# Kernel optimization log

Hardware: AMD Instinct MI355X
Metric: run time of the kernel (lower is better)

Reference implementation:

```python
import jax, jax.numpy as jnp
import numpy as np

N = 4096
SPECIES = 100
FEA = 64        # atom_emb_dim
NBR_FEA = 64    # num gaussians
MAX_NBRS = 12
LN_EPS = 1e-5

# GaussianSmearing constants: linspace(0, 8, 64)
_OFFSET = jnp.linspace(0.0, 8.0, NBR_FEA)
_COEFF = -0.5 / float(8.0 / (NBR_FEA - 1)) ** 2


def _uniform(key, shape, fan_in):
    s = 1.0 / np.sqrt(fan_in)
    return jax.random.uniform(key, shape, minval=-s, maxval=s, dtype=jnp.float32)


def setup_inputs() -> dict:
    key = jax.random.key(0)
    ks = jax.random.split(key, 20)
    lat_pred = jnp.eye(3, dtype=jnp.float32) * 8.0 + 0.2 * jax.random.normal(ks[0], (3, 3), dtype=jnp.float32)
    fracs_pred = jax.random.uniform(ks[1], (N, 3), dtype=jnp.float32)
    species_logits = jax.random.normal(ks[2], (N, SPECIES), dtype=jnp.float32)
    occ_logits = jax.random.normal(ks[3], (N,), dtype=jnp.float32)
    # params
    emb_w = _uniform(ks[4], (SPECIES, FEA), SPECIES)
    emb_b = _uniform(ks[5], (FEA,), SPECIES)
    in1 = 2 * FEA + NBR_FEA  # 192
    w1 = _uniform(ks[6], (in1, 2 * FEA), in1)
    b1 = _uniform(ks[7], (2 * FEA,), in1)
    g1 = jnp.ones((2 * FEA,), jnp.float32)
    be1 = jnp.zeros((2 * FEA,), jnp.float32)
    w2 = _uniform(ks[8], (in1, 2 * FEA), in1)
    b2 = _uniform(ks[9], (2 * FEA,), in1)
    g2 = jnp.ones((2 * FEA,), jnp.float32)
    be2 = jnp.zeros((2 * FEA,), jnp.float32)
    fc_w = _uniform(ks[10], (FEA, 1), FEA)
    fc_b = _uniform(ks[11], (1,), FEA)
    return dict(lat_pred=lat_pred, fracs_pred=fracs_pred, species_logits=species_logits,
                occ_logits=occ_logits, emb_w=emb_w, emb_b=emb_b,
                w1=w1, b1=b1, g1=g1, be1=be1, w2=w2, b2=b2, g2=g2, be2=be2,
                fc_w=fc_w, fc_b=fc_b)


def _layernorm(x, g, b):
    m = jnp.mean(x, axis=-1, keepdims=True)
    v = jnp.var(x, axis=-1, keepdims=True)
    return (x - m) * jax.lax.rsqrt(v + LN_EPS) * g + b


def _cgcnn_layer(atom, nbr_atom, nbr_fea, w, b, g, be):
    # atom: [N,F]; nbr_atom: [N,M,F]; nbr_fea: [N,M,K]
    n, m = nbr_atom.shape[:2]
    atom_exp = jnp.broadcast_to(atom[:, None, :], (n, m, atom.shape[-1]))
    total = jnp.concatenate([atom_exp, nbr_atom, nbr_fea], axis=2)  # [N,M,2F+K]
    z = _layernorm(total @ w + b, g, be)                            # [N,M,2F]
    nbr_filter, nbr_core = jnp.split(z, 2, axis=2)
    nbr_sumed = jnp.sum(jax.nn.sigmoid(nbr_filter) * jax.nn.softplus(nbr_core), axis=1)
    return jax.nn.softplus(atom + nbr_sumed)


def reference(lat_pred, fracs_pred, species_logits, occ_logits,
              emb_w, emb_b, w1, b1, g1, be1, w2, b2, g2, be2, fc_w, fc_b):
    species_probs = jax.nn.softmax(species_logits, axis=-1)
    atom_fea = species_probs @ emb_w + emb_b                         # [N,F]
    diff = fracs_pred[:, None, :] - fracs_pred[None, :, :]           # [N,N,3]
    diff = diff - jnp.round(diff)                                    # min-image
    cart = diff @ lat_pred                                           # [N,N,3]
    dist = jnp.linalg.norm(cart, axis=-1)                            # [N,N]
    dist = dist + jnp.eye(dist.shape[0], dtype=dist.dtype) * 100.0
    k = min(MAX_NBRS, dist.shape[1] - 1)
    neg_d, nbr_idx = jax.lax.top_k(-dist, k)                         # smallest k
    nbr_dist = -neg_d                                                # [N,k]
    nbr_fea = jnp.exp(_COEFF * (nbr_dist[..., None] - _OFFSET) ** 2) # [N,k,K]
    nbr_atom_fea = atom_fea[nbr_idx]                                 # [N,k,F]
    atom_fea = _cgcnn_layer(atom_fea, nbr_atom_fea, nbr_fea, w1, b1, g1, be1)
    atom_fea = _cgcnn_layer(atom_fea, nbr_atom_fea, nbr_fea, w2, b2, g2, be2)
    occ_probs = jax.nn.sigmoid(occ_logits)[:, None]                  # [N,1]
    graph_fea = jnp.sum(atom_fea * occ_probs, axis=0) / (jnp.sum(occ_probs) + 1e-6)
    return graph_fea @ fc_w + fc_b                                   # [1]
```

## Files before the change

### kernel.cpp

```cpp
#include <hip/hip_runtime.h>
#include <math.h>

#define N_ATOMS 4096
#define SPECIES 100
#define FEA 64
#define M_NBR 12

typedef unsigned short u16;
typedef __attribute__((ext_vector_type(8))) _Float16 f16x8;
typedef __attribute__((ext_vector_type(4))) float f32x4;

constexpr float LN_EPS = 1e-5f;
constexpr float GAUSS_COEFF = -31.0078125f;
constexpr float D2_INF = 3.4e38f;

__device__ __forceinline__ float sigmoidf_(float x){
    return __fdividef(1.0f, 1.0f + __expf(-x));
}
__device__ __forceinline__ float softplusf_(float x){
    return fmaxf(x, 0.0f) + __logf(1.0f + __expf(-fabsf(x)));
}
__device__ __forceinline__ u16 f16bits(_Float16 h){ return *(u16*)&h; }

__global__ __launch_bounds__(256) void k_setup(const float* __restrict__ fracs,
        const float* __restrict__ w1, const float* __restrict__ w2,
        const float* __restrict__ logits, const float* __restrict__ emb_w,
        const float* __restrict__ emb_b,
        float* __restrict__ fx, float* __restrict__ fy, float* __restrict__ fz,
        u16* __restrict__ wpk, float* __restrict__ atom0, u16* __restrict__ a0f){
    __shared__ float sE[4][SPECIES];
    int b = blockIdx.x, t = threadIdx.x;
    if (b < 192){
        int gid = b * 256 + t;
        int layer = gid / 24576;
        int e = gid % 24576;
        int k = e >> 7, n = e & 127;
        float x = (layer ? w2 : w1)[e];
        int mat = layer * 3 + (k >> 6);
        int kk = k & 63;
        int ch = kk >> 5, lg2 = (kk >> 3) & 3, i = kk & 7;
        int nt = n >> 4, lr2 = n & 15;
        wpk[mat * 8192 + ((ch * 8 + nt) * 64 + (lg2 * 16 + lr2)) * 8 + i] = f16bits((_Float16)x);
    } else if (b < 208){
        int j = (b - 192) * 256 + t;
        fx[j] = fracs[j*3+0];
        fy[j] = fracs[j*3+1];
        fz[j] = fracs[j*3+2];
    } else {
        int grp = t >> 6, f = t & 63;
        int a = (b - 208) * 4 + grp;
        const float* lg = logits + (long)a * SPECIES;
        float l0 = lg[f];
        float l1 = (f + 64 < SPECIES) ? lg[f + 64] : -1e30f;
        float mx = fmaxf(l0, l1);
        #pragma unroll
        for (int off = 32; off; off >>= 1) mx = fmaxf(mx, __shfl_xor(mx, off));
        float e0 = __expf(l0 - mx);
        float e1 = (f + 64 < SPECIES) ? __expf(l1 - mx) : 0.0f;
        sE[grp][f] = e0;
        if (f + 64 < SPECIES) sE[grp][64 + f] = e1;
        float sm = e0 + e1;
        #pragma unroll
        for (int off = 32; off; off >>= 1) sm += __shfl_xor(sm, off);
        __syncthreads();
        float acc = 0.0f;
        for (int s = 0; s < SPECIES; ++s) acc += sE[grp][s] * emb_w[s * FEA + f];
        float v = acc / sm + emb_b[f];
        atom0[(long)a * FEA + f] = v;
        a0f[a * FEA + f] = f16bits((_Float16)v);
    }
}

__global__ __launch_bounds__(256) void k_topk(const float* __restrict__ fx,
        const float* __restrict__ fy, const float* __restrict__ fz,
        const float* __restrict__ lat, int* __restrict__ nbr_idx,
        float* __restrict__ nbr_dist){
    __shared__ int   hist[256];
    __shared__ int   cnt;
    __shared__ float sThr;
    __shared__ float candD[256];
    __shared__ int   candI[256];
    int i = blockIdx.x, tid = threadIdx.x;
    hist[tid] = 0;
    if (tid == 0) cnt = 0;
    __syncthreads();
    float l00=lat[0],l01=lat[1],l02=lat[2];
    float l10=lat[3],l11=lat[4],l12=lat[5];
    float l20=lat[6],l21=lat[7],l22=lat[8];
    float xi = fx[i], yi = fy[i], zi = fz[i];
    float d2r[16];
    #pragma unroll
    for (int k = 0; k < 16; ++k){
        int j = tid + k * 256;
        float dx = xi - fx[j];
        float dy = yi - fy[j];
        float dz = zi - fz[j];
        dx -= rintf(dx); dy -= rintf(dy); dz -= rintf(dz);
        float cx = dx*l00 + dy*l10 + dz*l20;
        float cy = dx*l01 + dy*l11 + dz*l21;
        float cz = dx*l02 + dy*l12 + dz*l22;
        float d2 = cx*cx + cy*cy + cz*cz;
        if (j == i) d2 = D2_INF;
        d2r[k] = d2;
        if (d2 < 4.0f) atomicAdd(&hist[(int)(d2 * 64.0f)], 1);
    }
    __syncthreads();
    if (tid < 64){
        int s0 = hist[4*tid] + hist[4*tid+1] + hist[4*tid+2] + hist[4*tid+3];
        int sc = s0;
        #pragma unroll
        for (int off = 1; off < 64; off <<= 1){
            int o = __shfl_up(sc, off);
            if (tid >= off) sc += o;
        }
        unsigned long long mball = __ballot(sc >= M_NBR);
        if (mball == 0ULL){
            if (tid == 0) sThr = 1e30f;
        } else {
            int gbin = __ffsll(mball) - 1;
            if (tid == gbin){
                int c = sc - s0;
                float th = 4.0f;
                #pragma unroll
                for (int b = 0; b < 4; ++b){
                    c += hist[4*gbin + b];
                    if (c >= M_NBR){ th = (float)(4*gbin + b + 1) * (1.0f/64.0f); break; }
                }
                sThr = th;
            }
        }
    }
    __syncthreads();
    float thr = sThr;
    #pragma unroll
    for (int k = 0; k < 16; ++k){
        if (d2r[k] < thr){
            int p = atomicAdd(&cnt, 1);
            if (p < 256){ candD[p] = d2r[k]; candI[p] = tid + k * 256; }
        }
    }
    __syncthreads();
    int n = cnt < 256 ? cnt : 256;
    for (int c = tid; c < n; c += 256){
        float dv = candD[c]; int iv = candI[c];
        int rank = 0;
        for (int s = 0; s < n; ++s){
            float ds_ = candD[s]; int is_ = candI[s];
            rank += (ds_ < dv || (ds_ == dv && is_ < iv)) ? 1 : 0;
        }
        if (rank < M_NBR){
            nbr_idx[i * M_NBR + rank]  = iv;
            nbr_dist[i * M_NBR + rank] = sqrtf(dv);
        }
    }
}

__global__ __launch_bounds__(192) void k_fused(
        const float* __restrict__ atom0F, const u16* __restrict__ a0f,
        const int* __restrict__ nbr_idx, const float* __restrict__ nbr_dist,
        const u16* __restrict__ wpk,
        const float* __restrict__ b1, const float* __restrict__ g1, const float* __restrict__ be1,
        const float* __restrict__ b2, const float* __restrict__ g2, const float* __restrict__ be2,
        float* __restrict__ outF)
{
    __shared__ float sS1w[3][4][132];
    __shared__ float sS2w[3][4][132];
    __shared__ float prod[48][68];
    __shared__ float sSF[4][64];
    __shared__ u16   sSH[4][64];

    const int t = threadIdx.x;
    const int w = t >> 6, l = t & 63;
    const int lg = l >> 4, lr = l & 15;
    const int blk = blockIdx.x;
    const int row = blk * 48 + w * 16 + lr;

    const int nid = nbr_idx[row];
    f16x8 nfr[2];
    nfr[0] = *(const f16x8*)(a0f + nid * 64 + lg * 8);
    nfr[1] = *(const f16x8*)(a0f + nid * 64 + 32 + lg * 8);

    f16x8 saf[2];
    #pragma unroll
    for (int c = 0; c < 2; ++c)
        saf[c] = (lr < 4) ? *(const f16x8*)(a0f + (blk * 4 + lr) * 64 + c * 32 + lg * 8)
                          : (f16x8)0;

    const float* a0flat = atom0F + (long)blk * 256;
    float res0 = a0flat[t];
    float res1 = (t < 64) ? a0flat[192 + t] : 0.0f;

    float g1v[8], be1v[8];
    #pragma unroll
    for (int nt = 0; nt < 8; ++nt){
        int c = nt * 16 + lr;
        g1v[nt] = g1[c]; be1v[nt] = be1[c];
    }

    const float dist = nbr_dist[row];
    f16x8 ga[2];
    #pragma unroll
    for (int c = 0; c < 2; ++c)
        #pragma unroll
        for (int i = 0; i < 8; ++i){
            int k = c * 32 + lg * 8 + i;
            float dd = dist - (float)k * (8.0f / 63.0f);
            ga[c][i] = (_Float16)__expf(GAUSS_COEFF * dd * dd);
        }

    int aloc[4];
    #pragma unroll
    for (int rr = 0; rr < 4; ++rr)
        aloc[rr] = (w * 16 + lg * 4 + rr) / 12;

    const u16* ws1 = wpk;
    const u16* wn1 = wpk + 1 * 8192;
    const u16* wg1 = wpk + 2 * 8192;
    const u16* ws2 = wpk + 3 * 8192;
    const u16* wn2 = wpk + 4 * 8192;
    const u16* wg2 = wpk + 5 * 8192;

    {
        f32x4 a1[8];
        #pragma unroll
        for (int nt = 0; nt < 8; ++nt) a1[nt] = 0.0f;
        #pragma unroll
        for (int c = 0; c < 2; ++c)
            #pragma unroll
            for (int nt = 0; nt < 8; ++nt){
                const f16x8 b = *(const f16x8*)(ws1 + ((c * 8 + nt) * 64 + l) * 8);
                a1[nt] = __builtin_amdgcn_mfma_f32_16x16x32_f16(saf[c], b, a1[nt], 0, 0, 0);
            }
        if (lg == 0){
            #pragma unroll
            for (int nt = 0; nt < 8; ++nt)
                #pragma unroll
                for (int rr = 0; rr < 4; ++rr)
                    sS1w[w][rr][nt * 16 + lr] = a1[nt][rr] + b1[nt * 16 + lr];
        }
    }

    f32x4 acc[8];
    #pragma unroll
    for (int nt = 0; nt < 8; ++nt) acc[nt] = 0.0f;
    #pragma unroll
    for (int c = 0; c < 2; ++c)
        #pragma unroll
        for (int nt = 0; nt < 8; ++nt){
            const f16x8 bn = *(const f16x8*)(wn1 + ((c * 8 + nt) * 64 + l) * 8);
            acc[nt] = __builtin_amdgcn_mfma_f32_16x16x32_f16(nfr[c], bn, acc[nt], 0, 0, 0);
            const f16x8 bg = *(const f16x8*)(wg1 + ((c * 8 + nt) * 64 + l) * 8);
            acc[nt] = __builtin_amdgcn_mfma_f32_16x16x32_f16(ga[c], bg, acc[nt], 0, 0, 0);
        }

    {
        float s[4] = {0,0,0,0}, q[4] = {0,0,0,0};
        #pragma unroll
        for (int nt = 0; nt < 8; ++nt)
            #pragma unroll
            for (int rr = 0; rr < 4; ++rr){
                float v = acc[nt][rr] + sS1w[w][aloc[rr]][nt * 16 + lr];
                acc[nt][rr] = v;
                s[rr] += v; q[rr] += v * v;
            }
        #pragma unroll
        for (int rr = 0; rr < 4; ++rr){
            #pragma unroll
            for (int m = 1; m < 16; m <<= 1){
                s[rr] += __shfl_xor(s[rr], m);
                q[rr] += __shfl_xor(q[rr], m);
            }
        }
        #pragma unroll
        for (int rr = 0; rr < 4; ++rr){
            float mean = s[rr] * (1.0f / 128.0f);
            float var  = q[rr] * (1.0f / 128.0f) - mean * mean;
            float inv  = rsqrtf(var + LN_EPS);
            #pragma unroll
            for (int nt = 0; nt < 4; ++nt){
                float zf = (acc[nt][rr]     - mean) * inv * g1v[nt]     + be1v[nt];
                float zc = (acc[nt + 4][rr] - mean) * inv * g1v[nt + 4] + be1v[nt + 4];
                prod[w * 16 + lg * 4 + rr][nt * 16 + lr] = sigmoidf_(zf) * softplusf_(zc);
            }
        }
    }
    __syncthreads();

    {
        int a_ = t >> 6, c = t & 63;
        float sm = 0.0f;
        #pragma unroll
        for (int m = 0; m < 12; ++m) sm += prod[a_ * 12 + m][c];
        float o = softplusf_(res0 + sm);
        sSF[a_][c] = o;
        sSH[a_][c] = f16bits((_Float16)o);
        if (t < 64){
            float sm2 = 0.0f;
            #pragma unroll
            for (int m = 0; m < 12; ++m) sm2 += prod[36 + m][c];
            float o2 = softplusf_(res1 + sm2);
            sSF[3][c] = o2;
            sSH[3][c] = f16bits((_Float16)o2);
        }
    }
    __syncthreads();

    float g2v[8], be2v[8];
    #pragma unroll
    for (int nt = 0; nt < 8; ++nt){
        int c = nt * 16 + lr;
        g2v[nt] = g2[c]; be2v[nt] = be2[c];
    }

    {
        f16x8 af[2];
        #pragma unroll
        for (int c = 0; c < 2; ++c)
            af[c] = (lr < 4) ? *(const f16x8*)(&sSH[lr][c * 32 + lg * 8]) : (f16x8)0;
        f32x4 a2[8];
        #pragma unroll
        for (int nt = 0; nt < 8; ++nt) a2[nt] = 0.0f;
        #pragma unroll
        for (int c = 0; c < 2; ++c)
            #pragma unroll
            for (int nt = 0; nt < 8; ++nt){
                const f16x8 b = *(const f16x8*)(ws2 + ((c * 8 + nt) * 64 + l) * 8);
                a2[nt] = __builtin_amdgcn_mfma_f32_16x16x32_f16(af[c], b, a2[nt], 0, 0, 0);
            }
        if (lg == 0){
            #pragma unroll
            for (int nt = 0; nt < 8; ++nt)
                #pragma unroll
                for (int rr = 0; rr < 4; ++rr)
                    sS2w[w][rr][nt * 16 + lr] = a2[nt][rr] + b2[nt * 16 + lr];
        }
    }

    f32x4 acc2[8];
    #pragma unroll
    for (int nt = 0; nt < 8; ++nt) acc2[nt] = 0.0f;
    #pragma unroll
    for (int c = 0; c < 2; ++c)
        #pragma unroll
        for (int nt = 0; nt < 8; ++nt){
            const f16x8 bn = *(const f16x8*)(wn2 + ((c * 8 + nt) * 64 + l) * 8);
            acc2[nt] = __builtin_amdgcn_mfma_f32_16x16x32_f16(nfr[c], bn, acc2[nt], 0, 0, 0);
            const f16x8 bg = *(const f16x8*)(wg2 + ((c * 8 + nt) * 64 + l) * 8);
            acc2[nt] = __builtin_amdgcn_mfma_f32_16x16x32_f16(ga[c], bg, acc2[nt], 0, 0, 0);
        }

    {
        float s[4] = {0,0,0,0}, q[4] = {0,0,0,0};
        #pragma unroll
        for (int nt = 0; nt < 8; ++nt)
            #pragma unroll
            for (int rr = 0; rr < 4; ++rr){
                float v = acc2[nt][rr] + sS2w[w][aloc[rr]][nt * 16 + lr];
                acc2[nt][rr] = v;
                s[rr] += v; q[rr] += v * v;
            }
        #pragma unroll
        for (int rr = 0; rr < 4; ++rr){
            #pragma unroll
            for (int m = 1; m < 16; m <<= 1){
                s[rr] += __shfl_xor(s[rr], m);
                q[rr] += __shfl_xor(q[rr], m);
            }
        }
        #pragma unroll
        for (int rr = 0; rr < 4; ++rr){
            float mean = s[rr] * (1.0f / 128.0f);
            float var  = q[rr] * (1.0f / 128.0f) - mean * mean;
            float inv  = rsqrtf(var + LN_EPS);
            #pragma unroll
            for (int nt = 0; nt < 4; ++nt){
                float zf = (acc2[nt][rr]     - mean) * inv * g2v[nt]     + be2v[nt];
                float zc = (acc2[nt + 4][rr] - mean) * inv * g2v[nt + 4] + be2v[nt + 4];
                prod[w * 16 + lg * 4 + rr][nt * 16 + lr] = sigmoidf_(zf) * softplusf_(zc);
            }
        }
    }
    __syncthreads();

    {
        int a_ = t >> 6, c = t & 63;
        float sm = 0.0f;
        #pragma unroll
        for (int m = 0; m < 12; ++m) sm += prod[a_ * 12 + m][c];
        outF[(long)blk * 256 + t] = softplusf_(sSF[a_][c] + sm);
        if (t < 64){
            float sm2 = 0.0f;
            #pragma unroll
            for (int m = 0; m < 12; ++m) sm2 += prod[36 + m][c];
            outF[(long)blk * 256 + 192 + t] = softplusf_(sSF[3][c] + sm2);
        }
    }
}

__global__ __launch_bounds__(256) void k_partial(const float* __restrict__ atom,
        const float* __restrict__ occ, float* __restrict__ partials){
    int b = blockIdx.x, tid = threadIdx.x;
    int f = tid & 63, sub = tid >> 6;
    __shared__ float sAcc[256];
    float acc = 0.0f;
    for (int it = 0; it < 16; ++it){
        int a = b * 64 + sub + it * 4;
        float p = sigmoidf_(occ[a]);
        acc += atom[(long)a * FEA + f] * p;
    }
    sAcc[tid] = acc;
    __syncthreads();
    if (tid < 64){
        float s = sAcc[f] + sAcc[64 + f] + sAcc[128 + f] + sAcc[192 + f];
        partials[b * 65 + f] = s;
        float po = sigmoidf_(occ[b * 64 + f]);
        #pragma unroll
        for (int off = 32; off; off >>= 1) po += __shfl_down(po, off);
        if (f == 0) partials[b * 65 + 64] = po;
    }
}

__global__ __launch_bounds__(64) void k_final(const float* __restrict__ partials,
        const float* __restrict__ fc_w, const float* __restrict__ fc_b,
        float* __restrict__ out){
    int f = threadIdx.x;
    float num = 0.0f;
    for (int p = 0; p < 64; ++p) num += partials[p * 65 + f];
    float occs = partials[f * 65 + 64];
    #pragma unroll
    for (int off = 32; off; off >>= 1) occs += __shfl_down(occs, off);
    occs = __shfl(occs, 0);
    float gf = num / (occs + 1e-6f);
    float v = gf * fc_w[f];
    #pragma unroll
    for (int off = 32; off; off >>= 1) v += __shfl_down(v, off);
    if (f == 0) out[0] = v + fc_b[0];
}

extern "C" void kernel_launch(void* const* d_in, const int* in_sizes, int n_in,
                              void* d_out, int out_size, void* d_ws, size_t ws_size,
                              hipStream_t stream) {
    const float* lat    = (const float*)d_in[0];
    const float* fracs  = (const float*)d_in[1];
    const float* slog   = (const float*)d_in[2];
    const float* occ    = (const float*)d_in[3];
    const float* emb_w  = (const float*)d_in[4];
    const float* emb_b  = (const float*)d_in[5];
    const float* w1     = (const float*)d_in[6];
    const float* b1     = (const float*)d_in[7];
    const float* g1     = (const float*)d_in[8];
    const float* be1    = (const float*)d_in[9];
    const float* w2     = (const float*)d_in[10];
    const float* b2     = (const float*)d_in[11];
    const float* g2     = (const float*)d_in[12];
    const float* be2    = (const float*)d_in[13];
    const float* fc_w   = (const float*)d_in[14];
    const float* fc_b   = (const float*)d_in[15];
    float* out = (float*)d_out;

    char* ws = (char*)d_ws;
    auto alloc = [&](size_t bytes) -> void* {
        void* p = (void*)ws;
        ws += (bytes + 255) & ~(size_t)255;
        return p;
    };
    int*   nbr_idx  = (int*)  alloc((size_t)N_ATOMS * M_NBR * 4);
    float* nbr_dist = (float*)alloc((size_t)N_ATOMS * M_NBR * 4);
    float* atom0    = (float*)alloc((size_t)N_ATOMS * FEA * 4);
    float* atom1    = (float*)alloc((size_t)N_ATOMS * FEA * 4);
    u16*   a0f      = (u16*)  alloc((size_t)N_ATOMS * FEA * 2);
    u16*   wpk      = (u16*)  alloc((size_t)6 * 8192 * 2);
    float* fxa      = (float*)alloc((size_t)N_ATOMS * 4);
    float* fya      = (float*)alloc((size_t)N_ATOMS * 4);
    float* fza      = (float*)alloc((size_t)N_ATOMS * 4);
    float* partials = (float*)alloc((size_t)64 * 65 * 4);

    k_setup  <<<208 + N_ATOMS / 4, 256, 0, stream>>>(fracs, w1, w2, slog, emb_w, emb_b,
                fxa, fya, fza, wpk, atom0, a0f);
    k_topk   <<<N_ATOMS, 256, 0, stream>>>(fxa, fya, fza, lat, nbr_idx, nbr_dist);
    k_fused  <<<N_ATOMS / 4, 192, 0, stream>>>(atom0, a0f, nbr_idx, nbr_dist,
                wpk, b1, g1, be1, b2, g2, be2, atom1);
    k_partial<<<64, 256, 0, stream>>>(atom1, occ, partials);
    k_final  <<<1, 64, 0, stream>>>(partials, fc_w, fc_b, out);
}
```

Baseline: 62.13 us.

## Stage layer weights in LDS and process 8 atoms per block with two M-tiles

The fused CGCNN kernel now copies each layer's packed fp16 weights (48 KB) into shared memory once per block and reuses each B fragment across two 16-row M tiles per wave. Each block handles 8 atoms (96 neighbour rows) instead of 4, and the self-term GEMM runs on a single wave. The intent is to cut repeated global or L2 weight fetches and amortise them over twice the rows. In exchange it uses far more LDS per block, which lowers occupancy, and halves the grid to 512 blocks, adding extra barriers and weight-copy latency.

After: 63.58 us. +2.3%, slower.

```diff
diff --git a/kernel.cpp b/kernel.cpp
--- a/kernel.cpp
+++ b/kernel.cpp
@@ -163,64 +163,83 @@
         const float* __restrict__ b2, const float* __restrict__ g2, const float* __restrict__ be2,
         float* __restrict__ outF)
 {
-    __shared__ float sS1w[3][4][132];
-    __shared__ float sS2w[3][4][132];
-    __shared__ float prod[48][68];
-    __shared__ float sSF[4][64];
-    __shared__ u16   sSH[4][64];
+    __shared__ u16   wlds[24576];
+    __shared__ float prod[96][65];
+    __shared__ float sSF[8][64];
+    __shared__ u16   sSH[8][64];
+    __shared__ float sS[8][132];
 
     const int t = threadIdx.x;
     const int w = t >> 6, l = t & 63;
     const int lg = l >> 4, lr = l & 15;
     const int blk = blockIdx.x;
-    const int row = blk * 48 + w * 16 + lr;
-
-    const int nid = nbr_idx[row];
-    f16x8 nfr[2];
-    nfr[0] = *(const f16x8*)(a0f + nid * 64 + lg * 8);
-    nfr[1] = *(const f16x8*)(a0f + nid * 64 + 32 + lg * 8);
-
+
+    {
+        const float4* wsrc = (const float4*)wpk;
+        float4* wdst = (float4*)wlds;
+        #pragma unroll
+        for (int it = 0; it < 16; ++it)
+            wdst[it * 192 + t] = wsrc[it * 192 + t];
+    }
+
+    int nid[2]; float dist[2];
+    #pragma unroll
+    for (int mt = 0; mt < 2; ++mt){
+        int row = blk * 96 + w * 32 + mt * 16 + lr;
+        nid[mt]  = nbr_idx[row];
+        dist[mt] = nbr_dist[row];
+    }
+    f16x8 nfr[2][2];
+    #pragma unroll
+    for (int mt = 0; mt < 2; ++mt){
+        nfr[mt][0] = *(const f16x8*)(a0f + nid[mt] * 64 + lg * 8);
+        nfr[mt][1] = *(const f16x8*)(a0f + nid[mt] * 64 + 32 + lg * 8);
+    }
     f16x8 saf[2];
     #pragma unroll
     for (int c = 0; c < 2; ++c)
-        saf[c] = (lr < 4) ? *(const f16x8*)(a0f + (blk * 4 + lr) * 64 + c * 32 + lg * 8)
-                          : (f16x8)0;
-
-    const float* a0flat = atom0F + (long)blk * 256;
-    float res0 = a0flat[t];
-    float res1 = (t < 64) ? a0flat[192 + t] : 0.0f;
-
-    float g1v[8], be1v[8];
+        saf[c] = (w == 0 && lr < 8) ? *(const f16x8*)(a0f + (blk * 8 + lr) * 64 + c * 32 + lg * 8)
+                                    : (f16x8)0;
+    float res[3];
+    res[0] = atom0F[(long)blk * 512 + t];
+    res[1] = atom0F[(long)blk * 512 + 192 + t];
+    res[2] = (t < 128) ? atom0F[(long)blk * 512 + 384 + t] : 0.0f;
+
+    float g1v[8], be1v[8], g2v[8], be2v[8], b1v[8], b2v[8];
     #pragma unroll
     for (int nt = 0; nt < 8; ++nt){
         int c = nt * 16 + lr;
         g1v[nt] = g1[c]; be1v[nt] = be1[c];
-    }
-
-    const float dist = nbr_dist[row];
-    f16x8 ga[2];
-    #pragma unroll
-    for (int c = 0; c < 2; ++c)
-        #pragma unroll
-        for (int i = 0; i < 8; ++i){
-            int k = c * 32 + lg * 8 + i;
-            float dd = dist - (float)k * (8.0f / 63.0f);
-            ga[c][i] = (_Float16)__expf(GAUSS_COEFF * dd * dd);
-        }
-
-    int aloc[4];
-    #pragma unroll
-    for (int rr = 0; rr < 4; ++rr)
-        aloc[rr] = (w * 16 + lg * 4 + rr) / 12;
-
-    const u16* ws1 = wpk;
-    const u16* wn1 = wpk + 1 * 8192;
-    const u16* wg1 = wpk + 2 * 8192;
-    const u16* ws2 = wpk + 3 * 8192;
-    const u16* wn2 = wpk + 4 * 8192;
-    const u16* wg2 = wpk + 5 * 8192;
-
-    {
+        g2v[nt] = g2[c]; be2v[nt] = be2[c];
+        b1v[nt] = b1[c]; b2v[nt] = b2[c];
+    }
+
+    f16x8 ga[2][2];
+    #pragma unroll
+    for (int mt = 0; mt < 2; ++mt)
+        #pragma unroll
+        for (int c = 0; c < 2; ++c)
+            #pragma unroll
+            for (int i = 0; i < 8; ++i){
+                int k = c * 32 + lg * 8 + i;
+                float dd = dist[mt] - (float)k * (8.0f / 63.0f);
+                ga[mt][c][i] = (_Float16)__expf(GAUSS_COEFF * dd * dd);
+            }
+
+    int aloc[2][4];
+    #pragma unroll
+    for (int mt = 0; mt < 2; ++mt)
+        #pragma unroll
+        for (int rr = 0; rr < 4; ++rr)
+            aloc[mt][rr] = (w * 32 + mt * 16 + lg * 4 + rr) / 12;
+
+    const u16* wlS = wlds;
+    const u16* wlN = wlds + 8192;
+    const u16* wlG = wlds + 16384;
+
+    __syncthreads();
+
+    if (w == 0){
         f32x4 a1[8];
         #pragma unroll
         for (int nt = 0; nt < 8; ++nt) a1[nt] = 0.0f;
@@ -228,39 +247,45 @@
         for (int c = 0; c < 2; ++c)
             #pragma unroll
             for (int nt = 0; nt < 8; ++nt){
-                const f16x8 b = *(const f16x8*)(ws1 + ((c * 8 + nt) * 64 + l) * 8);
+                const f16x8 b = *(const f16x8*)(wlS + ((c * 8 + nt) * 64 + l) * 8);
                 a1[nt] = __builtin_amdgcn_mfma_f32_16x16x32_f16(saf[c], b, a1[nt], 0, 0, 0);
             }
-        if (lg == 0){
+        if (lg < 2){
             #pragma unroll
             for (int nt = 0; nt < 8; ++nt)
                 #pragma unroll
                 for (int rr = 0; rr < 4; ++rr)
-                    sS1w[w][rr][nt * 16 + lr] = a1[nt][rr] + b1[nt * 16 + lr];
-        }
-    }
-
-    f32x4 acc[8];
-    #pragma unroll
-    for (int nt = 0; nt < 8; ++nt) acc[nt] = 0.0f;
+                    sS[lg * 4 + rr][nt * 16 + lr] = a1[nt][rr] + b1v[nt];
+        }
+    }
+    f32x4 acc[2][8];
+    #pragma unroll
+    for (int mt = 0; mt < 2; ++mt)
+        #pragma unroll
+        for (int nt = 0; nt < 8; ++nt) acc[mt][nt] = 0.0f;
     #pragma unroll
     for (int c = 0; c < 2; ++c)
         #pragma unroll
         for (int nt = 0; nt < 8; ++nt){
-            const f16x8 bn = *(const f16x8*)(wn1 + ((c * 8 + nt) * 64 + l) * 8);
-            acc[nt] = __builtin_amdgcn_mfma_f32_16x16x32_f16(nfr[c], bn, acc[nt], 0, 0, 0);
-            const f16x8 bg = *(const f16x8*)(wg1 + ((c * 8 + nt) * 64 + l) * 8);
-            acc[nt] = __builtin_amdgcn_mfma_f32_16x16x32_f16(ga[c], bg, acc[nt], 0, 0, 0);
-        }
-
-    {
+            const f16x8 bn = *(const f16x8*)(wlN + ((c * 8 + nt) * 64 + l) * 8);
+            const f16x8 bg = *(const f16x8*)(wlG + ((c * 8 + nt) * 64 + l) * 8);
+            #pragma unroll
+            for (int mt = 0; mt < 2; ++mt){
+                acc[mt][nt] = __builtin_amdgcn_mfma_f32_16x16x32_f16(nfr[mt][c], bn, acc[mt][nt], 0, 0, 0);
+                acc[mt][nt] = __builtin_amdgcn_mfma_f32_16x16x32_f16(ga[mt][c],  bg, acc[mt][nt], 0, 0, 0);
+            }
+        }
+    __syncthreads();
+
+    #pragma unroll
+    for (int mt = 0; mt < 2; ++mt){
         float s[4] = {0,0,0,0}, q[4] = {0,0,0,0};
         #pragma unroll
         for (int nt = 0; nt < 8; ++nt)
             #pragma unroll
             for (int rr = 0; rr < 4; ++rr){
-                float v = acc[nt][rr] + sS1w[w][aloc[rr]][nt * 16 + lr];
-                acc[nt][rr] = v;
+                float v = acc[mt][nt][rr] + sS[aloc[mt][rr]][nt * 16 + lr];
+                acc[mt][nt][rr] = v;
                 s[rr] += v; q[rr] += v * v;
             }
         #pragma unroll
@@ -278,11 +303,18 @@
             float inv  = rsqrtf(var + LN_EPS);
             #pragma unroll
             for (int nt = 0; nt < 4; ++nt){
-                float zf = (acc[nt][rr]     - mean) * inv * g1v[nt]     + be1v[nt];
-                float zc = (acc[nt + 4][rr] - mean) * inv * g1v[nt + 4] + be1v[nt + 4];
-                prod[w * 16 + lg * 4 + rr][nt * 16 + lr] = sigmoidf_(zf) * softplusf_(zc);
-            }
-        }
+                float zf = (acc[mt][nt][rr]     - mean) * inv * g1v[nt]     + be1v[nt];
+                float zc = (acc[mt][nt + 4][rr] - mean) * inv * g1v[nt + 4] + be1v[nt + 4];
+                prod[w * 32 + mt * 16 + lg * 4 + rr][nt * 16 + lr] = sigmoidf_(zf) * softplusf_(zc);
+            }
+        }
+    }
+    {
+        const float4* wsrc2 = (const float4*)(wpk + 3 * 8192);
+        float4* wdst = (float4*)wlds;
+        #pragma unroll
+        for (int it = 0; it < 16; ++it)
+            wdst[it * 192 + t] = wsrc2[it * 192 + t];
     }
     __syncthreads();
 
@@ -291,32 +323,32 @@
         float sm = 0.0f;
         #pragma unroll
         for (int m = 0; m < 12; ++m) sm += prod[a_ * 12 + m][c];
-        float o = softplusf_(res0 + sm);
-        sSF[a_][c] = o;
-        sSH[a_][c] = f16bits((_Float16)o);
-        if (t < 64){
-            float sm2 = 0.0f;
-            #pragma unroll
-            for (int m = 0; m < 12; ++m) sm2 += prod[36 + m][c];
-            float o2 = softplusf_(res1 + sm2);
-            sSF[3][c] = o2;
-            sSH[3][c] = f16bits((_Float16)o2);
-        }
-    }
-    __syncthreads();
-
-    float g2v[8], be2v[8];
-    #pragma unroll
-    for (int nt = 0; nt < 8; ++nt){
-        int c = nt * 16 + lr;
-        g2v[nt] = g2[c]; be2v[nt] = be2[c];
-    }
-
-    {
+        float o = softplusf_(res[0] + sm);
+        sSF[a_][c] = o; sSH[a_][c] = f16bits((_Float16)o);
+
+        int i2 = t + 192; int a2_ = i2 >> 6, c2 = i2 & 63;
+        float sm2 = 0.0f;
+        #pragma unroll
+        for (int m = 0; m < 12; ++m) sm2 += prod[a2_ * 12 + m][c2];
+        float o2 = softplusf_(res[1] + sm2);
+        sSF[a2_][c2] = o2; sSH[a2_][c2] = f16bits((_Float16)o2);
+
+        if (t < 128){
+            int i3 = t + 384; int a3_ = i3 >> 6, c3 = i3 & 63;
+            float sm3 = 0.0f;
+            #pragma unroll
+            for (int m = 0; m < 12; ++m) sm3 += prod[a3_ * 12 + m][c3];
+            float o3 = softplusf_(res[2] + sm3);
+            sSF[a3_][c3] = o3; sSH[a3_][c3] = f16bits((_Float16)o3);
+        }
+    }
+    __syncthreads();
+
+    if (w == 1){
         f16x8 af[2];
         #pragma unroll
         for (int c = 0; c < 2; ++c)
-            af[c] = (lr < 4) ? *(const f16x8*)(&sSH[lr][c * 32 + lg * 8]) : (f16x8)0;
+            af[c] = (lr < 8) ? *(const f16x8*)(&sSH[lr][c * 32 + lg * 8]) : (f16x8)0;
         f32x4 a2[8];
         #pragma unroll
         for (int nt = 0; nt < 8; ++nt) a2[nt] = 0.0f;
@@ -324,39 +356,45 @@
         for (int c = 0; c < 2; ++c)
             #pragma unroll
             for (int nt = 0; nt < 8; ++nt){
-                const f16x8 b = *(const f16x8*)(ws2 + ((c * 8 + nt) * 64 + l) * 8);
+                const f16x8 b = *(const f16x8*)(wlS + ((c * 8 + nt) * 64 + l) * 8);
                 a2[nt] = __builtin_amdgcn_mfma_f32_16x16x32_f16(af[c], b, a2[nt], 0, 0, 0);
             }
-        if (lg == 0){
+        if (lg < 2){
             #pragma unroll
             for (int nt = 0; nt < 8; ++nt)
                 #pragma unroll
                 for (int rr = 0; rr < 4; ++rr)
-                    sS2w[w][rr][nt * 16 + lr] = a2[nt][rr] + b2[nt * 16 + lr];
-        }
-    }
-
-    f32x4 acc2[8];
-    #pragma unroll
-    for (int nt = 0; nt < 8; ++nt) acc2[nt] = 0.0f;
+                    sS[lg * 4 + rr][nt * 16 + lr] = a2[nt][rr] + b2v[nt];
+        }
+    }
+    f32x4 acc2[2][8];
+    #pragma unroll
+    for (int mt = 0; mt < 2; ++mt)
+        #pragma unroll
+        for (int nt = 0; nt < 8; ++nt) acc2[mt][nt] = 0.0f;
     #pragma unroll
     for (int c = 0; c < 2; ++c)
         #pragma unroll
         for (int nt = 0; nt < 8; ++nt){
-            const f16x8 bn = *(const f16x8*)(wn2 + ((c * 8 + nt) * 64 + l) * 8);
-            acc2[nt] = __builtin_amdgcn_mfma_f32_16x16x32_f16(nfr[c], bn, acc2[nt], 0, 0, 0);
-            const f16x8 bg = *(const f16x8*)(wg2 + ((c * 8 + nt) * 64 + l) * 8);
-            acc2[nt] = __builtin_amdgcn_mfma_f32_16x16x32_f16(ga[c], bg, acc2[nt], 0, 0, 0);
-        }
-
-    {
+            const f16x8 bn = *(const f16x8*)(wlN + ((c * 8 + nt) * 64 + l) * 8);
+            const f16x8 bg = *(const f16x8*)(wlG + ((c * 8 + nt) * 64 + l) * 8);
+            #pragma unroll
+            for (int mt = 0; mt < 2; ++mt){
+                acc2[mt][nt] = __builtin_amdgcn_mfma_f32_16x16x32_f16(nfr[mt][c], bn, acc2[mt][nt], 0, 0, 0);
+                acc2[mt][nt] = __builtin_amdgcn_mfma_f32_16x16x32_f16(ga[mt][c],  bg, acc2[mt][nt], 0, 0, 0);
+            }
+        }
+    __syncthreads();
+
+    #pragma unroll
+    for (int mt = 0; mt < 2; ++mt){
         float s[4] = {0,0,0,0}, q[4] = {0,0,0,0};
         #pragma unroll
         for (int nt = 0; nt < 8; ++nt)
             #pragma unroll
             for (int rr = 0; rr < 4; ++rr){
-                float v = acc2[nt][rr] + sS2w[w][aloc[rr]][nt * 16 + lr];
-                acc2[nt][rr] = v;
+                float v = acc2[mt][nt][rr] + sS[aloc[mt][rr]][nt * 16 + lr];
+                acc2[mt][nt][rr] = v;
                 s[rr] += v; q[rr] += v * v;
             }
         #pragma unroll
@@ -374,9 +412,9 @@
             float inv  = rsqrtf(var + LN_EPS);
             #pragma unroll
             for (int nt = 0; nt < 4; ++nt){
-                float zf = (acc2[nt][rr]     - mean) * inv * g2v[nt]     + be2v[nt];
-                float zc = (acc2[nt + 4][rr] - mean) * inv * g2v[nt + 4] + be2v[nt + 4];
-                prod[w * 16 + lg * 4 + rr][nt * 16 + lr] = sigmoidf_(zf) * softplusf_(zc);
+                float zf = (acc2[mt][nt][rr]     - mean) * inv * g2v[nt]     + be2v[nt];
+                float zc = (acc2[mt][nt + 4][rr] - mean) * inv * g2v[nt + 4] + be2v[nt + 4];
+                prod[w * 32 + mt * 16 + lg * 4 + rr][nt * 16 + lr] = sigmoidf_(zf) * softplusf_(zc);
             }
         }
     }
@@ -387,12 +425,20 @@
         float sm = 0.0f;
         #pragma unroll
         for (int m = 0; m < 12; ++m) sm += prod[a_ * 12 + m][c];
-        outF[(long)blk * 256 + t] = softplusf_(sSF[a_][c] + sm);
-        if (t < 64){
-            float sm2 = 0.0f;
-            #pragma unroll
-            for (int m = 0; m < 12; ++m) sm2 += prod[36 + m][c];
-            outF[(long)blk * 256 + 192 + t] = softplusf_(sSF[3][c] + sm2);
+        outF[(long)blk * 512 + t] = softplusf_(sSF[a_][c] + sm);
+
+        int i2 = t + 192; int a2_ = i2 >> 6, c2 = i2 & 63;
+        float sm2 = 0.0f;
+        #pragma unroll
+        for (int m = 0; m < 12; ++m) sm2 += prod[a2_ * 12 + m][c2];
+        outF[(long)blk * 512 + i2] = softplusf_(sSF[a2_][c2] + sm2);
+
+        if (t < 128){
+            int i3 = t + 384; int a3_ = i3 >> 6, c3 = i3 & 63;
+            float sm3 = 0.0f;
+            #pragma unroll
+            for (int m = 0; m < 12; ++m) sm3 += prod[a3_ * 12 + m][c3];
+            outF[(long)blk * 512 + i3] = softplusf_(sSF[a3_][c3] + sm3);
         }
     }
 }
@@ -478,7 +524,7 @@
     k_setup  <<<208 + N_ATOMS / 4, 256, 0, stream>>>(fracs, w1, w2, slog, emb_w, emb_b,
                 fxa, fya, fza, wpk, atom0, a0f);
     k_topk   <<<N_ATOMS, 256, 0, stream>>>(fxa, fya, fza, lat, nbr_idx, nbr_dist);
-    k_fused  <<<N_ATOMS / 4, 192, 0, stream>>>(atom0, a0f, nbr_idx, nbr_dist,
+    k_fused  <<<N_ATOMS / 8, 192, 0, stream>>>(atom0, a0f, nbr_idx, nbr_dist,
                 wpk, b1, g1, be1, b2, g2, be2, atom1);
     k_partial<<<64, 256, 0, stream>>>(atom1, occ, partials);
     k_final  <<<1, 64, 0, stream>>>(partials, fc_w, fc_b, out);
```

## Split fused CGCNN kernel into self-term precompute, edge packing, and GEMM kernels

Applied to the files above, without the earlier changes.

The single fused kernel is split into three. k_precomp computes the self-atom projection for all atoms with dense MFMA tiles instead of mostly zero-padded 4-row tiles. k_edges gathers neighbour features and computes the Gaussian expansion into a packed fp16 edge matrix X. k_gemm then loads its MFMA operands from X with contiguous reads. This moves the gather latency and transcendental work out of the GEMM kernel, at the cost of two extra launches and a round trip of roughly 12 MB of intermediate data through global memory.

Result: slower. 71.35 us (+14.8%).

```diff
diff --git a/kernel.cpp b/kernel.cpp
--- a/kernel.cpp
+++ b/kernel.cpp
@@ -155,17 +155,67 @@
     }
 }
 
-__global__ __launch_bounds__(192) void k_fused(
-        const float* __restrict__ atom0F, const u16* __restrict__ a0f,
+__global__ __launch_bounds__(64) void k_precomp(const u16* __restrict__ a0f,
+        const u16* __restrict__ wpk, const float* __restrict__ b1,
+        float* __restrict__ S1){
+    const int l = threadIdx.x;
+    const int lg = l >> 4, lr = l & 15;
+    const int blk = blockIdx.x;
+    f16x8 af[2];
+    #pragma unroll
+    for (int c = 0; c < 2; ++c)
+        af[c] = *(const f16x8*)(a0f + (blk * 16 + lr) * 64 + c * 32 + lg * 8);
+    f32x4 acc[8];
+    #pragma unroll
+    for (int nt = 0; nt < 8; ++nt) acc[nt] = 0.0f;
+    #pragma unroll
+    for (int c = 0; c < 2; ++c)
+        #pragma unroll
+        for (int nt = 0; nt < 8; ++nt){
+            const f16x8 b = *(const f16x8*)(wpk + ((c * 8 + nt) * 64 + l) * 8);
+            acc[nt] = __builtin_amdgcn_mfma_f32_16x16x32_f16(af[c], b, acc[nt], 0, 0, 0);
+        }
+    #pragma unroll
+    for (int nt = 0; nt < 8; ++nt)
+        #pragma unroll
+        for (int rr = 0; rr < 4; ++rr)
+            S1[(blk * 16 + lg * 4 + rr) * 128 + nt * 16 + lr] = acc[nt][rr] + b1[nt * 16 + lr];
+}
+
+__global__ __launch_bounds__(256) void k_edges(const u16* __restrict__ a0f,
         const int* __restrict__ nbr_idx, const float* __restrict__ nbr_dist,
-        const u16* __restrict__ wpk,
-        const float* __restrict__ b1, const float* __restrict__ g1, const float* __restrict__ be1,
-        const float* __restrict__ b2, const float* __restrict__ g2, const float* __restrict__ be2,
+        u16* __restrict__ X){
+    const int blk = blockIdx.x, t = threadIdx.x;
+    const int c = (t >> 6) & 3;
+    const int lane = t & 63;
+    const int sub = lane >> 4;
+    const int row = blk * 16 + (lane & 15);
+    f16x8 v;
+    if (c < 2){
+        v = *(const f16x8*)(a0f + nbr_idx[row] * 64 + c * 32 + sub * 8);
+    } else {
+        float d = nbr_dist[row];
+        #pragma unroll
+        for (int i = 0; i < 8; ++i){
+            int k = (c - 2) * 32 + sub * 8 + i;
+            float dd = d - (float)k * (8.0f / 63.0f);
+            v[i] = (_Float16)__expf(GAUSS_COEFF * dd * dd);
+        }
+    }
+    *(f16x8*)(X + ((long)blk * 256 + t) * 8) = v;
+}
+
+__global__ __launch_bounds__(192) void k_gemm(
+        const float* __restrict__ atom0F, const u16* __restrict__ X,
+        const u16* __restrict__ wpk, const float* __restrict__ S1g,
+        const float* __restrict__ b2,
+        const float* __restrict__ g1, const float* __restrict__ be1,
+        const float* __restrict__ g2, const float* __restrict__ be2,
         float* __restrict__ outF)
 {
-    __shared__ float sS1w[3][4][132];
+    __shared__ float sS1[4][132];
     __shared__ float sS2w[3][4][132];
-    __shared__ float prod[48][68];
+    __shared__ float prod[48][65];
     __shared__ float sSF[4][64];
     __shared__ u16   sSH[4][64];
 
@@ -173,85 +223,47 @@
     const int w = t >> 6, l = t & 63;
     const int lg = l >> 4, lr = l & 15;
     const int blk = blockIdx.x;
-    const int row = blk * 48 + w * 16 + lr;
-
-    const int nid = nbr_idx[row];
-    f16x8 nfr[2];
-    nfr[0] = *(const f16x8*)(a0f + nid * 64 + lg * 8);
-    nfr[1] = *(const f16x8*)(a0f + nid * 64 + 32 + lg * 8);
-
-    f16x8 saf[2];
-    #pragma unroll
-    for (int c = 0; c < 2; ++c)
-        saf[c] = (lr < 4) ? *(const f16x8*)(a0f + (blk * 4 + lr) * 64 + c * 32 + lg * 8)
-                          : (f16x8)0;
-
-    const float* a0flat = atom0F + (long)blk * 256;
-    float res0 = a0flat[t];
-    float res1 = (t < 64) ? a0flat[192 + t] : 0.0f;
-
-    float g1v[8], be1v[8];
+
+    if (t < 128){
+        int a_ = t >> 5, c4 = (t & 31) << 2;
+        *(float4*)(&sS1[a_][c4]) = *(const float4*)(S1g + (long)(blk * 4 + a_) * 128 + c4);
+    }
+
+    f16x8 af[4];
+    #pragma unroll
+    for (int c = 0; c < 4; ++c)
+        af[c] = *(const f16x8*)(X + (((long)(blk * 3 + w) * 4 + c) * 64 + l) * 8);
+
+    float res0 = atom0F[(long)blk * 256 + t];
+    float res1 = (t < 64) ? atom0F[(long)blk * 256 + 192 + t] : 0.0f;
+
+    float g1v[8], be1v[8], g2v[8], be2v[8], b2v[8];
     #pragma unroll
     for (int nt = 0; nt < 8; ++nt){
         int c = nt * 16 + lr;
         g1v[nt] = g1[c]; be1v[nt] = be1[c];
-    }
-
-    const float dist = nbr_dist[row];
-    f16x8 ga[2];
-    #pragma unroll
-    for (int c = 0; c < 2; ++c)
-        #pragma unroll
-        for (int i = 0; i < 8; ++i){
-            int k = c * 32 + lg * 8 + i;
-            float dd = dist - (float)k * (8.0f / 63.0f);
-            ga[c][i] = (_Float16)__expf(GAUSS_COEFF * dd * dd);
-        }
+        g2v[nt] = g2[c]; be2v[nt] = be2[c];
+        b2v[nt] = b2[c];
+    }
 
     int aloc[4];
     #pragma unroll
     for (int rr = 0; rr < 4; ++rr)
         aloc[rr] = (w * 16 + lg * 4 + rr) / 12;
 
-    const u16* ws1 = wpk;
-    const u16* wn1 = wpk + 1 * 8192;
-    const u16* wg1 = wpk + 2 * 8192;
-    const u16* ws2 = wpk + 3 * 8192;
-    const u16* wn2 = wpk + 4 * 8192;
-    const u16* wg2 = wpk + 5 * 8192;
-
-    {
-        f32x4 a1[8];
-        #pragma unroll
-        for (int nt = 0; nt < 8; ++nt) a1[nt] = 0.0f;
-        #pragma unroll
-        for (int c = 0; c < 2; ++c)
-            #pragma unroll
-            for (int nt = 0; nt < 8; ++nt){
-                const f16x8 b = *(const f16x8*)(ws1 + ((c * 8 + nt) * 64 + l) * 8);
-                a1[nt] = __builtin_amdgcn_mfma_f32_16x16x32_f16(saf[c], b, a1[nt], 0, 0, 0);
-            }
-        if (lg == 0){
-            #pragma unroll
-            for (int nt = 0; nt < 8; ++nt)
-                #pragma unroll
-                for (int rr = 0; rr < 4; ++rr)
-                    sS1w[w][rr][nt * 16 + lr] = a1[nt][rr] + b1[nt * 16 + lr];
-        }
-    }
-
     f32x4 acc[8];
     #pragma unroll
     for (int nt = 0; nt < 8; ++nt) acc[nt] = 0.0f;
     #pragma unroll
-    for (int c = 0; c < 2; ++c)
+    for (int c = 0; c < 4; ++c)
         #pragma unroll
         for (int nt = 0; nt < 8; ++nt){
-            const f16x8 bn = *(const f16x8*)(wn1 + ((c * 8 + nt) * 64 + l) * 8);
-            acc[nt] = __builtin_amdgcn_mfma_f32_16x16x32_f16(nfr[c], bn, acc[nt], 0, 0, 0);
-            const f16x8 bg = *(const f16x8*)(wg1 + ((c * 8 + nt) * 64 + l) * 8);
-            acc[nt] = __builtin_amdgcn_mfma_f32_16x16x32_f16(ga[c], bg, acc[nt], 0, 0, 0);
-        }
+            const u16* bm = (c < 2)
+                ? wpk + 1 * 8192 + ((c * 8 + nt) * 64 + l) * 8
+                : wpk + 2 * 8192 + (((c - 2) * 8 + nt) * 64 + l) * 8;
+            acc[nt] = __builtin_amdgcn_mfma_f32_16x16x32_f16(af[c], *(const f16x8*)bm, acc[nt], 0, 0, 0);
+        }
+    __syncthreads();
 
     {
         float s[4] = {0,0,0,0}, q[4] = {0,0,0,0};
@@ -259,7 +271,7 @@
         for (int nt = 0; nt < 8; ++nt)
             #pragma unroll
             for (int rr = 0; rr < 4; ++rr){
-                float v = acc[nt][rr] + sS1w[w][aloc[rr]][nt * 16 + lr];
+                float v = acc[nt][rr] + sS1[aloc[rr]][nt * 16 + lr];
                 acc[nt][rr] = v;
                 s[rr] += v; q[rr] += v * v;
             }
@@ -292,31 +304,22 @@
         #pragma unroll
         for (int m = 0; m < 12; ++m) sm += prod[a_ * 12 + m][c];
         float o = softplusf_(res0 + sm);
-        sSF[a_][c] = o;
-        sSH[a_][c] = f16bits((_Float16)o);
+        sSF[a_][c] = o; sSH[a_][c] = f16bits((_Float16)o);
         if (t < 64){
             float sm2 = 0.0f;
             #pragma unroll
             for (int m = 0; m < 12; ++m) sm2 += prod[36 + m][c];
             float o2 = softplusf_(res1 + sm2);
-            sSF[3][c] = o2;
-            sSH[3][c] = f16bits((_Float16)o2);
-        }
-    }
-    __syncthreads();
-
-    float g2v[8], be2v[8];
-    #pragma unroll
-    for (int nt = 0; nt < 8; ++nt){
-        int c = nt * 16 + lr;
-        g2v[nt] = g2[c]; be2v[nt] = be2[c];
-    }
+            sSF[3][c] = o2; sSH[3][c] = f16bits((_Float16)o2);
+        }
+    }
+    __syncthreads();
 
     {
-        f16x8 af[2];
+        f16x8 af2[2];
         #pragma unroll
         for (int c = 0; c < 2; ++c)
-            af[c] = (lr < 4) ? *(const f16x8*)(&sSH[lr][c * 32 + lg * 8]) : (f16x8)0;
+            af2[c] = (lr < 4) ? *(const f16x8*)(&sSH[lr][c * 32 + lg * 8]) : (f16x8)0;
         f32x4 a2[8];
         #pragma unroll
         for (int nt = 0; nt < 8; ++nt) a2[nt] = 0.0f;
@@ -324,15 +327,15 @@
         for (int c = 0; c < 2; ++c)
             #pragma unroll
             for (int nt = 0; nt < 8; ++nt){
-                const f16x8 b = *(const f16x8*)(ws2 + ((c * 8 + nt) * 64 + l) * 8);
-                a2[nt] = __builtin_amdgcn_mfma_f32_16x16x32_f16(af[c], b, a2[nt], 0, 0, 0);
+                const f16x8 b = *(const f16x8*)(wpk + 3 * 8192 + ((c * 8 + nt) * 64 + l) * 8);
+                a2[nt] = __builtin_amdgcn_mfma_f32_16x16x32_f16(af2[c], b, a2[nt], 0, 0, 0);
             }
         if (lg == 0){
             #pragma unroll
             for (int nt = 0; nt < 8; ++nt)
                 #pragma unroll
                 for (int rr = 0; rr < 4; ++rr)
-                    sS2w[w][rr][nt * 16 + lr] = a2[nt][rr] + b2[nt * 16 + lr];
+                    sS2w[w][rr][nt * 16 + lr] = a2[nt][rr] + b2v[nt];
         }
     }
 
@@ -340,13 +343,13 @@
     #pragma unroll
     for (int nt = 0; nt < 8; ++nt) acc2[nt] = 0.0f;
     #pragma unroll
-    for (int c = 0; c < 2; ++c)
+    for (int c = 0; c < 4; ++c)
         #pragma unroll
         for (int nt = 0; nt < 8; ++nt){
-            const f16x8 bn = *(const f16x8*)(wn2 + ((c * 8 + nt) * 64 + l) * 8);
-            acc2[nt] = __builtin_amdgcn_mfma_f32_16x16x32_f16(nfr[c], bn, acc2[nt], 0, 0, 0);
-            const f16x8 bg = *(const f16x8*)(wg2 + ((c * 8 + nt) * 64 + l) * 8);
-            acc2[nt] = __builtin_amdgcn_mfma_f32_16x16x32_f16(ga[c], bg, acc2[nt], 0, 0, 0);
+            const u16* bm = (c < 2)
+                ? wpk + 4 * 8192 + ((c * 8 + nt) * 64 + l) * 8
+                : wpk + 5 * 8192 + (((c - 2) * 8 + nt) * 64 + l) * 8;
+            acc2[nt] = __builtin_amdgcn_mfma_f32_16x16x32_f16(af[c], *(const f16x8*)bm, acc2[nt], 0, 0, 0);
         }
 
     {
@@ -470,6 +473,8 @@
     float* atom1    = (float*)alloc((size_t)N_ATOMS * FEA * 4);
     u16*   a0f      = (u16*)  alloc((size_t)N_ATOMS * FEA * 2);
     u16*   wpk      = (u16*)  alloc((size_t)6 * 8192 * 2);
+    float* S1       = (float*)alloc((size_t)N_ATOMS * 128 * 4);
+    u16*   X        = (u16*)  alloc((size_t)N_ATOMS * M_NBR * 128 * 2);
     float* fxa      = (float*)alloc((size_t)N_ATOMS * 4);
     float* fya      = (float*)alloc((size_t)N_ATOMS * 4);
     float* fza      = (float*)alloc((size_t)N_ATOMS * 4);
@@ -478,8 +483,10 @@
     k_setup  <<<208 + N_ATOMS / 4, 256, 0, stream>>>(fracs, w1, w2, slog, emb_w, emb_b,
                 fxa, fya, fza, wpk, atom0, a0f);
     k_topk   <<<N_ATOMS, 256, 0, stream>>>(fxa, fya, fza, lat, nbr_idx, nbr_dist);
-    k_fused  <<<N_ATOMS / 4, 192, 0, stream>>>(atom0, a0f, nbr_idx, nbr_dist,
-                wpk, b1, g1, be1, b2, g2, be2, atom1);
+    k_precomp<<<N_ATOMS / 16, 64, 0, stream>>>(a0f, wpk, b1, S1);
+    k_edges  <<<N_ATOMS * M_NBR / 16, 256, 0, stream>>>(a0f, nbr_idx, nbr_dist, X);
+    k_gemm   <<<N_ATOMS / 4, 192, 0, stream>>>(atom0, X, wpk, S1, b2,
+                g1, be1, g2, be2, atom1);
     k_partial<<<64, 256, 0, stream>>>(atom1, occ, partials);
     k_final  <<<1, 64, 0, stream>>>(partials, fc_w, fc_b, out);
 }
```
